# Optimization experiments

Measured on AMD Instinct MI355X. Metric: run time of the kernel, lower is better.

The kernel has to match this reference:

```python
import jax, jax.numpy as jnp
import numpy as np

B, FIN, FOUT, N_TASKS = 256, 1024, 512, 20
FOUT2 = 2 * FOUT  # ConditionalLinear is built with 2*fout


def setup_inputs() -> dict:
    key = jax.random.key(0)
    k1, k2, k3 = jax.random.split(key, 3)
    x = jax.random.normal(k1, (B, FIN), dtype=jnp.float32)
    task_id = jax.random.randint(k2, (B,), 0, N_TASKS)
    # Embedding table [n_tasks, fin*2*fout]; kaiming_normal(fan_out) std = sqrt(2/fout2)
    std = np.sqrt(2.0 / FOUT2).astype(np.float32)
    W = jax.random.normal(k3, (N_TASKS, FIN * FOUT2), dtype=jnp.float32) * std
    return {"x": x, "task_id": task_id, "W": W}


def reference(x, task_id, W):
    Bsz, fin = x.shape
    fout2 = W.shape[1] // fin
    # task-conditional weight gather: [B, 2*fout, fin]
    w = W[task_id].reshape(Bsz, fout2, fin)
    # per-sample matvec (torch.bmm with x.unsqueeze(2))
    logits = jnp.einsum('boi,bi->bo', w, x).reshape(Bsz, fout2 // 2, 2)
    # BinaryGumbelSoftmax eval path: h = 1 - argmax(softmax(logits)) = 1 - argmax(logits)
    h = 1.0 - jnp.argmax(logits, axis=-1).astype(logits.dtype)
    return (h, logits)
```

## Files before the change

### kernel.cpp

```cpp
#include <hip/hip_runtime.h>

#define FIN   1024
#define FOUT2 1024
#define NTASK 20
#define NRG   256
#define NSLOT 2
#define NW    (NTASK * NRG * NSLOT)
#define HOFF  (256 * 512)

__global__ __launch_bounds__(64, 2)
void cond_linear_kernel(const float* __restrict__ x,
                        const int* __restrict__ task_id,
                        const float* __restrict__ W,
                        float* __restrict__ out) {
    __shared__ int sh_ord[64];

    const int lane = threadIdx.x;
    const int bid  = blockIdx.x;
    const int orig = (bid & 7) * (NW / 8) + (bid >> 3);
    const int t    = orig >> 9;
    const int r2   = orig & 511;
    const int rg   = r2 >> 1;
    const int slot = r2 & 1;
    const int o0   = rg * 4;

    const float* Wt = W + (size_t)t * (FOUT2 * FIN);
    float4 wr[4][4];
    #pragma unroll
    for (int r = 0; r < 4; ++r) {
        const float4* wp = (const float4*)(Wt + (size_t)(o0 + r) * FIN);
        #pragma unroll
        for (int p = 0; p < 4; ++p)
            wr[r][p] = wp[p * 64 + lane];
    }

    const int4 ids = ((const int4*)task_id)[lane];
    const unsigned long long m0 = __ballot(ids.x == t);
    const unsigned long long m1 = __ballot(ids.y == t);
    const unsigned long long m2 = __ballot(ids.z == t);
    const unsigned long long m3 = __ballot(ids.w == t);
    const unsigned long long below = (1ull << lane) - 1ull;
    int rank = __popcll(m0 & below) + __popcll(m1 & below)
             + __popcll(m2 & below) + __popcll(m3 & below);
    if (ids.x == t) sh_ord[rank] = 4 * lane + 0;
    rank += (int)((m0 >> lane) & 1);
    if (ids.y == t) sh_ord[rank] = 4 * lane + 1;
    rank += (int)((m1 >> lane) & 1);
    if (ids.z == t) sh_ord[rank] = 4 * lane + 2;
    rank += (int)((m2 >> lane) & 1);
    if (ids.w == t) sh_ord[rank] = 4 * lane + 3;

    const int n = __popcll(m0) + __popcll(m1) + __popcll(m2) + __popcll(m3);
    const int half = (n + 1) >> 1;
    const int i0 = slot ? half : 0;
    const int i1 = slot ? n    : half;
    if (i0 >= i1) return;

    #pragma unroll
    for (int r = 0; r < 4; ++r)
        #pragma unroll
        for (int p = 0; p < 4; ++p)
            asm volatile("" : "+v"(wr[r][p].x), "+v"(wr[r][p].y),
                              "+v"(wr[r][p].z), "+v"(wr[r][p].w));

    const bool hi32 = (lane & 32) != 0;
    const bool hi16 = (lane & 16) != 0;
    const bool hi8  = (lane & 8)  != 0;

    int sa = sh_ord[i0];
    int sb = sh_ord[(i0 + 1 < i1) ? i0 + 1 : i1 - 1];
    float4 xa[4], xb[4];
    #pragma unroll
    for (int p = 0; p < 4; ++p)
        xa[p] = ((const float4*)(x + (size_t)sa * FIN))[p * 64 + lane];
    #pragma unroll
    for (int p = 0; p < 4; ++p)
        xb[p] = ((const float4*)(x + (size_t)sb * FIN))[p * 64 + lane];

    for (int i = i0; i < i1; i += 2) {
        const int ina = (i + 2 < i1) ? i + 2 : i1 - 1;
        const int inb = (i + 3 < i1) ? i + 3 : i1 - 1;
        const int na_s = sh_ord[ina];
        const int nb_s = sh_ord[inb];
        float4 na[4], nb[4];
        #pragma unroll
        for (int p = 0; p < 4; ++p)
            na[p] = ((const float4*)(x + (size_t)na_s * FIN))[p * 64 + lane];
        #pragma unroll
        for (int p = 0; p < 4; ++p)
            nb[p] = ((const float4*)(x + (size_t)nb_s * FIN))[p * 64 + lane];

        float a0 = 0.f, a1 = 0.f, a2 = 0.f, a3 = 0.f;
        float b0 = 0.f, b1 = 0.f, b2 = 0.f, b3 = 0.f;
        #pragma unroll
        for (int p = 0; p < 4; ++p) {
            const float4 u = xa[p];
            const float4 v = xb[p];
            a0 += wr[0][p].x * u.x + wr[0][p].y * u.y + wr[0][p].z * u.z + wr[0][p].w * u.w;
            a1 += wr[1][p].x * u.x + wr[1][p].y * u.y + wr[1][p].z * u.z + wr[1][p].w * u.w;
            a2 += wr[2][p].x * u.x + wr[2][p].y * u.y + wr[2][p].z * u.z + wr[2][p].w * u.w;
            a3 += wr[3][p].x * u.x + wr[3][p].y * u.y + wr[3][p].z * u.z + wr[3][p].w * u.w;
            b0 += wr[0][p].x * v.x + wr[0][p].y * v.y + wr[0][p].z * v.z + wr[0][p].w * v.w;
            b1 += wr[1][p].x * v.x + wr[1][p].y * v.y + wr[1][p].z * v.z + wr[1][p].w * v.w;
            b2 += wr[2][p].x * v.x + wr[2][p].y * v.y + wr[2][p].z * v.z + wr[2][p].w * v.w;
            b3 += wr[3][p].x * v.x + wr[3][p].y * v.y + wr[3][p].z * v.z + wr[3][p].w * v.w;
        }

        const float t0 = a0 + __shfl_xor(a0, 32, 64);
        const float t1 = a1 + __shfl_xor(a1, 32, 64);
        const float t2 = a2 + __shfl_xor(a2, 32, 64);
        const float t3 = a3 + __shfl_xor(a3, 32, 64);
        const float t4 = b0 + __shfl_xor(b0, 32, 64);
        const float t5 = b1 + __shfl_xor(b1, 32, 64);
        const float t6 = b2 + __shfl_xor(b2, 32, 64);
        const float t7 = b3 + __shfl_xor(b3, 32, 64);
        float w0 = hi32 ? t4 : t0;
        float w1 = hi32 ? t5 : t1;
        float w2 = hi32 ? t6 : t2;
        float w3 = hi32 ? t7 : t3;
        w0 += __shfl_xor(w0, 16, 64);
        w1 += __shfl_xor(w1, 16, 64);
        w2 += __shfl_xor(w2, 16, 64);
        w3 += __shfl_xor(w3, 16, 64);
        float u0 = hi16 ? w2 : w0;
        float u1 = hi16 ? w3 : w1;
        u0 += __shfl_xor(u0, 8, 64);
        u1 += __shfl_xor(u1, 8, 64);
        float z = hi8 ? u1 : u0;
        z += __shfl_xor(z, 4, 64);
        z += __shfl_xor(z, 2, 64);
        z += __shfl_xor(z, 1, 64);
        const float zp = __shfl_xor(z, 8, 64);

        const int r_id = (hi8 ? 1 : 0) + (hi16 ? 2 : 0);
        const int s_idx = hi32 ? sb : sa;
        if ((lane & 7) == 0) {
            out[HOFF + (size_t)s_idx * FOUT2 + o0 + r_id] = z;
            if (!hi8) {
                out[(size_t)s_idx * (FOUT2 / 2) + (o0 >> 1) + (hi16 ? 1 : 0)]
                    = (z >= zp) ? 1.0f : 0.0f;
            }
        }

        sa = na_s; sb = nb_s;
        #pragma unroll
        for (int p = 0; p < 4; ++p) { xa[p] = na[p]; xb[p] = nb[p]; }
    }
}

extern "C" void kernel_launch(void* const* d_in, const int* in_sizes, int n_in,
                              void* d_out, int out_size, void* d_ws, size_t ws_size,
                              hipStream_t stream) {
    const float* x       = (const float*)d_in[0];
    const int*   task_id = (const int*)d_in[1];
    const float* W       = (const float*)d_in[2];
    float*       out     = (float*)d_out;

    dim3 grid(NW);
    dim3 block(64);
    hipLaunchKernelGGL(cond_linear_kernel, grid, block, 0, stream,
                       x, task_id, W, out);
}
```

Measured before the change: 29.44 us.

## Process eight output rows per wave to raise x reuse

Result: slower. 45.06 us (+53.1%).

```diff
diff --git a/kernel.cpp b/kernel.cpp
--- a/kernel.cpp
+++ b/kernel.cpp
@@ -3,7 +3,7 @@
 #define FIN   1024
 #define FOUT2 1024
 #define NTASK 20
-#define NRG   256
+#define NRG   128
 #define NSLOT 2
 #define NW    (NTASK * NRG * NSLOT)
 #define HOFF  (256 * 512)
@@ -18,16 +18,16 @@
     const int lane = threadIdx.x;
     const int bid  = blockIdx.x;
     const int orig = (bid & 7) * (NW / 8) + (bid >> 3);
-    const int t    = orig >> 9;
-    const int r2   = orig & 511;
+    const int t    = orig >> 8;
+    const int r2   = orig & 255;
     const int rg   = r2 >> 1;
     const int slot = r2 & 1;
-    const int o0   = rg * 4;
+    const int o0   = rg * 8;
 
     const float* Wt = W + (size_t)t * (FOUT2 * FIN);
-    float4 wr[4][4];
+    float4 wr[8][4];
     #pragma unroll
-    for (int r = 0; r < 4; ++r) {
+    for (int r = 0; r < 8; ++r) {
         const float4* wp = (const float4*)(Wt + (size_t)(o0 + r) * FIN);
         #pragma unroll
         for (int p = 0; p < 4; ++p)
@@ -57,7 +57,7 @@
     if (i0 >= i1) return;
 
     #pragma unroll
-    for (int r = 0; r < 4; ++r)
+    for (int r = 0; r < 8; ++r)
         #pragma unroll
         for (int p = 0; p < 4; ++p)
             asm volatile("" : "+v"(wr[r][p].x), "+v"(wr[r][p].y),
@@ -66,6 +66,7 @@
     const bool hi32 = (lane & 32) != 0;
     const bool hi16 = (lane & 16) != 0;
     const bool hi8  = (lane & 8)  != 0;
+    const bool hi4  = (lane & 4)  != 0;
 
     int sa = sh_ord[i0];
     int sb = sh_ord[(i0 + 1 < i1) ? i0 + 1 : i1 - 1];
@@ -90,54 +91,56 @@
         for (int p = 0; p < 4; ++p)
             nb[p] = ((const float4*)(x + (size_t)nb_s * FIN))[p * 64 + lane];
 
-        float a0 = 0.f, a1 = 0.f, a2 = 0.f, a3 = 0.f;
-        float b0 = 0.f, b1 = 0.f, b2 = 0.f, b3 = 0.f;
+        float aacc[8], bacc[8];
+        #pragma unroll
+        for (int r = 0; r < 8; ++r) { aacc[r] = 0.f; bacc[r] = 0.f; }
+
         #pragma unroll
         for (int p = 0; p < 4; ++p) {
             const float4 u = xa[p];
             const float4 v = xb[p];
-            a0 += wr[0][p].x * u.x + wr[0][p].y * u.y + wr[0][p].z * u.z + wr[0][p].w * u.w;
-            a1 += wr[1][p].x * u.x + wr[1][p].y * u.y + wr[1][p].z * u.z + wr[1][p].w * u.w;
-            a2 += wr[2][p].x * u.x + wr[2][p].y * u.y + wr[2][p].z * u.z + wr[2][p].w * u.w;
-            a3 += wr[3][p].x * u.x + wr[3][p].y * u.y + wr[3][p].z * u.z + wr[3][p].w * u.w;
-            b0 += wr[0][p].x * v.x + wr[0][p].y * v.y + wr[0][p].z * v.z + wr[0][p].w * v.w;
-            b1 += wr[1][p].x * v.x + wr[1][p].y * v.y + wr[1][p].z * v.z + wr[1][p].w * v.w;
-            b2 += wr[2][p].x * v.x + wr[2][p].y * v.y + wr[2][p].z * v.z + wr[2][p].w * v.w;
-            b3 += wr[3][p].x * v.x + wr[3][p].y * v.y + wr[3][p].z * v.z + wr[3][p].w * v.w;
+            #pragma unroll
+            for (int r = 0; r < 8; ++r) {
+                aacc[r] += wr[r][p].x * u.x + wr[r][p].y * u.y
+                         + wr[r][p].z * u.z + wr[r][p].w * u.w;
+                bacc[r] += wr[r][p].x * v.x + wr[r][p].y * v.y
+                         + wr[r][p].z * v.z + wr[r][p].w * v.w;
+            }
         }
 
-        const float t0 = a0 + __shfl_xor(a0, 32, 64);
-        const float t1 = a1 + __shfl_xor(a1, 32, 64);
-        const float t2 = a2 + __shfl_xor(a2, 32, 64);
-        const float t3 = a3 + __shfl_xor(a3, 32, 64);
-        const float t4 = b0 + __shfl_xor(b0, 32, 64);
-        const float t5 = b1 + __shfl_xor(b1, 32, 64);
-        const float t6 = b2 + __shfl_xor(b2, 32, 64);
-        const float t7 = b3 + __shfl_xor(b3, 32, 64);
-        float w0 = hi32 ? t4 : t0;
-        float w1 = hi32 ? t5 : t1;
-        float w2 = hi32 ? t6 : t2;
-        float w3 = hi32 ? t7 : t3;
-        w0 += __shfl_xor(w0, 16, 64);
-        w1 += __shfl_xor(w1, 16, 64);
-        w2 += __shfl_xor(w2, 16, 64);
-        w3 += __shfl_xor(w3, 16, 64);
-        float u0 = hi16 ? w2 : w0;
-        float u1 = hi16 ? w3 : w1;
-        u0 += __shfl_xor(u0, 8, 64);
-        u1 += __shfl_xor(u1, 8, 64);
-        float z = hi8 ? u1 : u0;
-        z += __shfl_xor(z, 4, 64);
+        float t_[16];
+        #pragma unroll
+        for (int r = 0; r < 8; ++r) {
+            t_[r]     = aacc[r] + __shfl_xor(aacc[r], 32, 64);
+            t_[8 + r] = bacc[r] + __shfl_xor(bacc[r], 32, 64);
+        }
+        float w_[8];
+        #pragma unroll
+        for (int r = 0; r < 8; ++r) w_[r] = hi32 ? t_[8 + r] : t_[r];
+        #pragma unroll
+        for (int r = 0; r < 8; ++r) w_[r] += __shfl_xor(w_[r], 16, 64);
+        float u_[4];
+        #pragma unroll
+        for (int j = 0; j < 4; ++j) u_[j] = hi16 ? w_[j + 4] : w_[j];
+        #pragma unroll
+        for (int j = 0; j < 4; ++j) u_[j] += __shfl_xor(u_[j], 8, 64);
+        float v_[2];
+        #pragma unroll
+        for (int j = 0; j < 2; ++j) v_[j] = hi8 ? u_[j + 2] : u_[j];
+        #pragma unroll
+        for (int j = 0; j < 2; ++j) v_[j] += __shfl_xor(v_[j], 4, 64);
+        float z = hi4 ? v_[1] : v_[0];
         z += __shfl_xor(z, 2, 64);
         z += __shfl_xor(z, 1, 64);
-        const float zp = __shfl_xor(z, 8, 64);
+        const float zp = __shfl_xor(z, 4, 64);
 
-        const int r_id = (hi8 ? 1 : 0) + (hi16 ? 2 : 0);
+        const int r_id  = (hi4 ? 1 : 0) + (hi8 ? 2 : 0) + (hi16 ? 4 : 0);
         const int s_idx = hi32 ? sb : sa;
-        if ((lane & 7) == 0) {
+        if ((lane & 3) == 0) {
             out[HOFF + (size_t)s_idx * FOUT2 + o0 + r_id] = z;
-            if (!hi8) {
-                out[(size_t)s_idx * (FOUT2 / 2) + (o0 >> 1) + (hi16 ? 1 : 0)]
+            if (!hi4) {
+                out[(size_t)s_idx * (FOUT2 / 2) + (o0 >> 1)
+                    + (hi16 ? 2 : 0) + (hi8 ? 1 : 0)]
                     = (z >= zp) ? 1.0f : 0.0f;
             }
         }
```
